# Kernel optimization log

Measured on AMD Instinct MI355X. Metric: run time of the kernel, lower is better.

Reference implementation:

```python
import jax, jax.numpy as jnp
import numpy as np

# Static configuration (mirrors init_kwargs / forward defaults)
KERNEL = 128          # WW
INDEX_BACK = 32768    # number of highest-frequency bins discarded
PADDING = 0           # padding_count (padding=None in forward)

def next_power2(x):
    return int(2 ** np.ceil(np.log2(x)))

def setup_inputs() -> dict:
    key = jax.random.key(0)
    k1, k2, k3 = jax.random.split(key, 3)
    N, C, W = 32, 8, 65536
    F = 16
    x = jax.random.normal(k1, (N, C, W), dtype=jnp.float32)
    weight = jax.random.normal(k2, (F, C, KERNEL), dtype=jnp.float32) * 0.1
    bias = jax.random.normal(k3, (F,), dtype=jnp.float32)
    return {"x": x, "weight": weight, "bias": bias}

def reference(x, weight, bias):
    # x: [N, C, W], weight: [F, C, WW], bias: [F]
    N, C, W = x.shape
    F, _, WW = weight.shape
    pad = PADDING
    out_W = W - WW + 1 + 2 * pad
    # fft size sized to also hold the backward dout correlation, then next pow2
    init_fft_size_input = W + 2 * pad + 2 * (WW - 1)
    init_fft_size_dout = out_W + 2 * (WW - 1)
    init_fft_size = next_power2(max(init_fft_size_input, init_fft_size_dout))
    half = init_fft_size // 2 + 1

    # rfft with implicit zero-padding to init_fft_size (input left-padded by `pad`)
    x_p = jnp.pad(x, ((0, 0), (0, 0), (pad, 0)))
    xfft = jnp.fft.rfft(x_p, n=init_fft_size, axis=-1)      # [N, C, half]
    yfft = jnp.fft.rfft(weight, n=init_fft_size, axis=-1)   # [F, C, half]

    # spectral compression: drop the INDEX_BACK highest-frequency bins
    keep = half - INDEX_BACK
    xfft = xfft[..., :keep]
    yfft = yfft[..., :keep]

    # cross-correlation in frequency domain (torch conv == correlation),
    # summing over input channels C in the spectrum (linearity of irfft)
    outfft = jnp.einsum('nck,fck->nfk', xfft, jnp.conj(yfft))  # [N, F, keep]

    # zero-pad discarded high frequencies back and invert
    outfft = jnp.pad(outfft, ((0, 0), (0, 0), (0, half - keep)))
    out = jnp.fft.irfft(outfft, n=init_fft_size, axis=-1)[..., :out_W]  # [N, F, out_W]

    out = out + bias[None, :, None]
    return out
```

## Files before the change

### kernel.cpp

```cpp
#include <hip/hip_runtime.h>

namespace {

constexpr int NFFT  = 65536;
constexpr int KEEPK = 32768;
constexpr int OUTW  = 65409;
constexpr size_t YBYTES = (size_t)128 * 32769 * 8;

typedef float2 cplx;

__device__ __forceinline__ cplx cmk(float x, float y){ return make_float2(x, y); }
__device__ __forceinline__ cplx cadd(cplx a, cplx b){ return cmk(a.x+b.x, a.y+b.y); }
__device__ __forceinline__ cplx csub(cplx a, cplx b){ return cmk(a.x-b.x, a.y-b.y); }
__device__ __forceinline__ cplx cmul(cplx a, cplx b){ return cmk(a.x*b.x - a.y*b.y, a.x*b.y + a.y*b.x); }
__device__ __forceinline__ cplx cmulj(cplx a, cplx b){
  return cmk(a.x*b.x + a.y*b.y, a.y*b.x - a.x*b.y); }

template<int DIR>
__device__ __forceinline__ void dft16(cplx v[16]) {
  const float C1 = 0.92387953251128674f;
  const float S1 = 0.38268343236508977f;
  const float C2 = 0.70710678118654752f;
  const float WR[16]  = {1.f, C1, C2, S1, 0.f, -S1, -C2, -C1, -1.f, -C1, -C2, -S1, 0.f, S1, C2, C1};
  const float WIF[16] = {0.f, -S1, -C2, -C1, -1.f, -C1, -C2, -S1, 0.f, S1, C2, C1, 1.f, C1, C2, S1};
  cplx s[16];
  #pragma unroll
  for (int n2 = 0; n2 < 4; ++n2) {
    cplx a = v[n2], b = v[n2+4], c = v[n2+8], d = v[n2+12];
    cplx ac = cadd(a,c), am = csub(a,c), bd = cadd(b,d), bm = csub(b,d);
    cplx x0 = cadd(ac, bd), x2 = csub(ac, bd), x1, x3;
    if (DIR == -1) { x1 = cmk(am.x + bm.y, am.y - bm.x); x3 = cmk(am.x - bm.y, am.y + bm.x); }
    else           { x1 = cmk(am.x - bm.y, am.y + bm.x); x3 = cmk(am.x + bm.y, am.y - bm.x); }
    s[0*4+n2] = x0;
    {
      int e1 = (n2*1) & 15, e2 = (n2*2) & 15, e3 = (n2*3) & 15;
      cplx w1 = cmk(WR[e1], (DIR==-1)? WIF[e1] : -WIF[e1]);
      cplx w2 = cmk(WR[e2], (DIR==-1)? WIF[e2] : -WIF[e2]);
      cplx w3 = cmk(WR[e3], (DIR==-1)? WIF[e3] : -WIF[e3]);
      s[1*4+n2] = cmul(x1, w1);
      s[2*4+n2] = cmul(x2, w2);
      s[3*4+n2] = cmul(x3, w3);
    }
  }
  #pragma unroll
  for (int t1 = 0; t1 < 4; ++t1) {
    cplx a = s[t1*4+0], b = s[t1*4+1], c = s[t1*4+2], d = s[t1*4+3];
    cplx ac = cadd(a,c), am = csub(a,c), bd = cadd(b,d), bm = csub(b,d);
    cplx x0 = cadd(ac,bd), x2 = csub(ac,bd), x1, x3;
    if (DIR == -1) { x1 = cmk(am.x + bm.y, am.y - bm.x); x3 = cmk(am.x - bm.y, am.y + bm.x); }
    else           { x1 = cmk(am.x - bm.y, am.y + bm.x); x3 = cmk(am.x + bm.y, am.y - bm.x); }
    v[t1+0] = x0; v[t1+4] = x1; v[t1+8] = x2; v[t1+12] = x3;
  }
}

template<int DIR>
__global__ __launch_bounds__(256)
void fft_pass_a(const cplx* __restrict__ in, long inStride, int inLen,
                cplx* __restrict__ T) {
  int blk = blockIdx.x;
  int seq = blk >> 4;
  int B0  = (blk & 15) << 4;
  int t = threadIdx.x;
  __shared__ cplx tile[16][260];
  {
    const cplx* src = in + (long)seq * inStride;
    int cb = t & 15, rg = t >> 4;
    #pragma unroll
    for (int i = 0; i < 16; ++i) {
      int a = i*16 + rg;
      int sIdx = a*256 + B0 + cb;
      cplx v = (sIdx < inLen) ? src[sIdx] : cmk(0.f, 0.f);
      tile[cb][a] = v;
    }
  }
  __syncthreads();
  int cc = t >> 4, j = t & 15;
  cplx x[16];
  #pragma unroll
  for (int a1 = 0; a1 < 16; ++a1) x[a1] = tile[cc][a1*16 + j];
  dft16<DIR>(x);
  {
    float sn, cs;
    __sincosf((float)DIR * 6.28318530717958648f * (float)j * (1.0f/256.0f), &sn, &cs);
    cplx r = cmk(cs, sn), cur = r;
    #pragma unroll
    for (int t1 = 1; t1 < 16; ++t1) { x[t1] = cmul(x[t1], cur); cur = cmul(cur, r); }
  }
  __syncthreads();
  #pragma unroll
  for (int t1 = 0; t1 < 16; ++t1) tile[cc][t1*16 + ((j + t1) & 15)] = x[t1];
  __syncthreads();
  #pragma unroll
  for (int a2 = 0; a2 < 16; ++a2) x[a2] = tile[cc][j*16 + ((a2 + j) & 15)];
  dft16<DIR>(x);
  int b = B0 + cc;
  cplx* dst = T + (long)seq * NFFT + (long)b * 256;
  {
    float sn, cs;
    __sincosf((float)DIR * 6.28318530717958648f * (float)(b*j) * (1.0f/65536.0f), &sn, &cs);
    cplx cur = cmk(cs, sn);
    __sincosf((float)DIR * 6.28318530717958648f * (float)b * (1.0f/4096.0f), &sn, &cs);
    cplx stp = cmk(cs, sn);
    #pragma unroll
    for (int t2 = 0; t2 < 16; ++t2) {
      dst[j + 16*t2] = cmul(x[t2], cur);
      cur = cmul(cur, stp);
    }
  }
}

template<int DIR, int MODE>
__global__ __launch_bounds__(256)
void fft_pass_b(const cplx* __restrict__ T, cplx* __restrict__ outZ,
                float* __restrict__ outR, const float* __restrict__ bias,
                int seqBase) {
  int blk = blockIdx.x;
  int seq = blk >> 4;
  int K0  = (blk & 15) << 4;
  int t = threadIdx.x;
  __shared__ cplx tile[16][260];
  {
    const cplx* src = T + (long)seq * NFFT;
    int ck = t & 15, rg = t >> 4;
    #pragma unroll
    for (int i = 0; i < 16; ++i) {
      int b = i*16 + rg;
      tile[ck][b] = src[b*256 + K0 + ck];
    }
  }
  __syncthreads();
  int cc = t >> 4, j = t & 15;
  cplx x[16];
  #pragma unroll
  for (int a1 = 0; a1 < 16; ++a1) x[a1] = tile[cc][a1*16 + j];
  dft16<DIR>(x);
  {
    float sn, cs;
    __sincosf((float)DIR * 6.28318530717958648f * (float)j * (1.0f/256.0f), &sn, &cs);
    cplx r = cmk(cs, sn), cur = r;
    #pragma unroll
    for (int t1 = 1; t1 < 16; ++t1) { x[t1] = cmul(x[t1], cur); cur = cmul(cur, r); }
  }
  __syncthreads();
  #pragma unroll
  for (int t1 = 0; t1 < 16; ++t1) tile[cc][t1*16 + ((j + t1) & 15)] = x[t1];
  __syncthreads();
  #pragma unroll
  for (int a2 = 0; a2 < 16; ++a2) x[a2] = tile[cc][j*16 + ((a2 + j) & 15)];
  dft16<DIR>(x);
  __syncthreads();
  #pragma unroll
  for (int t2 = 0; t2 < 16; ++t2) tile[cc][j + 16*t2] = x[t2];
  __syncthreads();
  int ck2 = t & 15, rg2 = t >> 4;
  if (MODE == 0) {
    cplx* dst = outZ + (long)seq * NFFT + K0 + ck2;
    #pragma unroll
    for (int i = 0; i < 16; ++i) {
      int k2 = i*16 + rg2;
      dst[256*k2] = tile[ck2][k2];
    }
  } else {
    const float sc = 1.0f / 65536.0f;
    int gseq = seqBase + seq;
    float bf = bias[gseq & 15];
    float* dst = outR + (long)gseq * OUTW;
    #pragma unroll
    for (int i = 0; i < 16; ++i) {
      int k2 = i*16 + rg2;
      int s  = K0 + ck2 + 256*k2;
      int tp = 2*s;
      cplx v = tile[ck2][k2];
      if (tp < OUTW)     dst[tp]   = v.x * sc + bf;
      if (tp + 1 < OUTW) dst[tp+1] = v.y * sc + bf;
    }
  }
}

__global__ __launch_bounds__(256)
void weight_spec(const float* __restrict__ wgt, cplx* __restrict__ Y) {
  int seq = blockIdx.y;
  int k = blockIdx.x * 256 + threadIdx.x;
  __shared__ float wt[128];
  if (threadIdx.x < 128) wt[threadIdx.x] = wgt[seq * 128 + threadIdx.x];
  __syncthreads();
  if (k > KEEPK) return;
  float sn, cs;
  __sincosf(-3.14159265358979324f * (float)k * (1.0f/65536.0f), &sn, &cs);
  cplx r  = cmk(cs, sn);
  cplx r2 = cmul(r, r);
  cplx r4 = cmul(r2, r2);
  cplx r8 = cmul(r4, r4);
  cplx av[8];
  #pragma unroll
  for (int v = 0; v < 8; ++v) av[v] = cmk(0.f, 0.f);
  cplx C = cmk(1.f, 0.f);
  #pragma unroll
  for (int u = 0; u < 16; ++u) {
    #pragma unroll
    for (int v = 0; v < 8; ++v) {
      float w = wt[u*8 + v];
      av[v].x += w * C.x;
      av[v].y += w * C.y;
    }
    C = cmul(C, r8);
  }
  cplx acc = av[7];
  #pragma unroll
  for (int v = 6; v >= 0; --v) acc = cadd(av[v], cmul(r, acc));
  Y[(long)seq * 32769 + k] = acc;
}

__global__ __launch_bounds__(256)
void mac_pack(const cplx* __restrict__ Zx, const cplx* __restrict__ Yspec,
              cplx* __restrict__ Zout, int Bn) {
  int K0 = blockIdx.x * 32;
  int tid = threadIdx.x;
  int kk = tid & 31;
  int ng = tid >> 5;
  int k = K0 + kk;
  __shared__ cplx Yt[16][8][32];
  for (int e = tid; e < 16*8*32; e += 256) {
    int f = e >> 8;
    int c = (e >> 5) & 7;
    int q = e & 31;
    int kg = K0 + q;
    Yt[f][c][q] = (kg <= KEEPK) ? Yspec[(long)(f*8 + c) * 32769 + kg] : cmk(0.f, 0.f);
  }
  __syncthreads();
  if (k > KEEPK) return;
  float sn, cs;
  __sincosf(-3.14159265358979324f * (float)k * (1.0f/65536.0f), &sn, &cs);
  cplx w  = cmk(cs, sn);
  cplx wp = cmk(cs, -sn);
  int nPerG = (Bn + 7) >> 3;
  for (int nn = 0; nn < nPerG; ++nn) {
    int ln = ng * nPerG + nn;
    if (ln >= Bn) break;
    cplx X[8];
    #pragma unroll
    for (int c = 0; c < 8; ++c) {
      const cplx* Z = Zx + (long)(ln*8 + c) * NFFT;
      cplx zk = Z[k];
      cplx zm = Z[(NFFT - k) & (NFFT - 1)];
      cplx E = cmk(0.5f*(zk.x + zm.x), 0.5f*(zk.y - zm.y));
      cplx D = cmk(zk.x - zm.x, zk.y + zm.y);
      cplx O = cmk(0.5f*D.y, -0.5f*D.x);
      X[c] = cadd(E, cmul(w, O));
    }
    #pragma unroll
    for (int f = 0; f < 16; ++f) {
      cplx S = cmk(0.f, 0.f);
      #pragma unroll
      for (int c = 0; c < 8; ++c) S = cadd(S, cmulj(X[c], Yt[f][c][kk]));
      cplx* Zo = Zout + (long)(ln*16 + f) * NFFT;
      if (k == KEEPK) {
        Zo[k] = cmk(S.x, -S.y);
      } else {
        cplx E2 = cmk(0.5f*S.x, 0.5f*S.y);
        cplx O2 = cmul(wp, E2);
        Zo[k] = cmk(E2.x - O2.y, E2.y + O2.x);
        if (k > 0)
          Zo[NFFT - k] = cmk(E2.x + O2.y, O2.x - E2.y);
      }
    }
  }
}

}

extern "C" void kernel_launch(void* const* d_in, const int* in_sizes, int n_in,
                              void* d_out, int out_size, void* d_ws, size_t ws_size,
                              hipStream_t stream) {
  const cplx*  x    = (const cplx*)d_in[0];
  const float* wgt  = (const float*)d_in[1];
  const float* bias = (const float*)d_in[2];
  float* out = (float*)d_out;

  static const int BnOpt[5] = {16, 8, 4, 2, 1};
  int ti = 4;
  for (int i = 0; i < 5; ++i) {
    size_t zxb = (size_t)BnOpt[i] * 8  * NFFT * sizeof(cplx);
    size_t zob = (size_t)BnOpt[i] * 16 * NFFT * sizeof(cplx);
    if (YBYTES + zxb + 2 * zob <= ws_size) { ti = i; break; }
  }
  const int Bn = BnOpt[ti];
  const size_t zxb = (size_t)Bn * 8  * NFFT * sizeof(cplx);
  const size_t zob = (size_t)Bn * 16 * NFFT * sizeof(cplx);

  char* ws = (char*)d_ws;
  cplx* Y  = (cplx*)ws;
  cplx* Zx = (cplx*)(ws + YBYTES);
  cplx* Zo = (cplx*)(ws + YBYTES + zxb);
  cplx* T  = (cplx*)(ws + YBYTES + zxb + zob);

  weight_spec<<<dim3(129, 128), dim3(256), 0, stream>>>(wgt, Y);

  for (int n0 = 0; n0 < 32; n0 += Bn) {
    int sx = Bn * 8;
    int so = Bn * 16;
    fft_pass_a<-1><<<dim3(sx*16), dim3(256), 0, stream>>>(x + (long)n0*8*32768, 32768, 32768, T);
    fft_pass_b<-1,0><<<dim3(sx*16), dim3(256), 0, stream>>>(T, Zx, (float*)nullptr, (const float*)nullptr, 0);
    mac_pack<<<dim3(1025), dim3(256), 0, stream>>>(Zx, Y, Zo, Bn);
    fft_pass_a<1><<<dim3(so*16), dim3(256), 0, stream>>>(Zo, 65536, 65536, T);
    fft_pass_b<1,1><<<dim3(so*16), dim3(256), 0, stream>>>(T, (cplx*)nullptr, out, bias, n0*16);
  }
}
```

Measured before the change: 662.3 us.

## Fuse forward FFT pass B, spectral MAC and inverse FFT pass A into one kernel

```diff
diff --git a/kernel.cpp b/kernel.cpp
--- a/kernel.cpp
+++ b/kernel.cpp
@@ -3,9 +3,8 @@
 namespace {
 
 constexpr int NFFT  = 65536;
-constexpr int KEEPK = 32768;
 constexpr int OUTW  = 65409;
-constexpr size_t YBYTES = (size_t)128 * 32769 * 8;
+constexpr size_t Y2BYTES = (size_t)256 * 129 * 128 * 8;
 
 typedef float2 cplx;
 
@@ -94,7 +93,7 @@
   for (int a2 = 0; a2 < 16; ++a2) x[a2] = tile[cc][j*16 + ((a2 + j) & 15)];
   dft16<DIR>(x);
   int b = B0 + cc;
-  cplx* dst = T + (long)seq * NFFT + (long)b * 256;
+  cplx* dst = T + (long)seq * NFFT + b;
   {
     float sn, cs;
     __sincosf((float)DIR * 6.28318530717958648f * (float)(b*j) * (1.0f/65536.0f), &sn, &cs);
@@ -103,7 +102,7 @@
     cplx stp = cmk(cs, sn);
     #pragma unroll
     for (int t2 = 0; t2 < 16; ++t2) {
-      dst[j + 16*t2] = cmul(x[t2], cur);
+      dst[(j + 16*t2) * 256] = cmul(x[t2], cur);
       cur = cmul(cur, stp);
     }
   }
@@ -178,90 +177,199 @@
 }
 
 __global__ __launch_bounds__(256)
-void weight_spec(const float* __restrict__ wgt, cplx* __restrict__ Y) {
-  int seq = blockIdx.y;
-  int k = blockIdx.x * 256 + threadIdx.x;
-  __shared__ float wt[128];
-  if (threadIdx.x < 128) wt[threadIdx.x] = wgt[seq * 128 + threadIdx.x];
-  __syncthreads();
-  if (k > KEEPK) return;
-  float sn, cs;
-  __sincosf(-3.14159265358979324f * (float)k * (1.0f/65536.0f), &sn, &cs);
-  cplx r  = cmk(cs, sn);
-  cplx r2 = cmul(r, r);
-  cplx r4 = cmul(r2, r2);
-  cplx r8 = cmul(r4, r4);
-  cplx av[8];
-  #pragma unroll
-  for (int v = 0; v < 8; ++v) av[v] = cmk(0.f, 0.f);
-  cplx C = cmk(1.f, 0.f);
-  #pragma unroll
-  for (int u = 0; u < 16; ++u) {
-    #pragma unroll
-    for (int v = 0; v < 8; ++v) {
-      float w = wt[u*8 + v];
-      av[v].x += w * C.x;
-      av[v].y += w * C.y;
-    }
-    C = cmul(C, r8);
-  }
-  cplx acc = av[7];
-  #pragma unroll
-  for (int v = 6; v >= 0; --v) acc = cadd(av[v], cmul(r, acc));
-  Y[(long)seq * 32769 + k] = acc;
+void weight_spec(const float* __restrict__ wgt, cplx* __restrict__ Y2) {
+  const int k1 = blockIdx.x;
+  const int fg = blockIdx.y;
+  const int t  = threadIdx.x;
+  __shared__ float wt[16][129];
+  for (int e = t; e < 16*128; e += 256)
+    wt[e >> 7][e & 127] = wgt[(fg*16 + (e >> 7))*128 + (e & 127)];
+  __syncthreads();
+  const int fcL = t & 15;
+  const int fc  = fg*16 + fcL;
+  for (int m = t >> 4; m < 129; m += 16) {
+    int k = k1 + 256*m;
+    if (k > 32768) break;
+    float sn, cs;
+    __sincosf(-3.14159265358979324f * (float)k * (1.0f/65536.0f), &sn, &cs);
+    cplx r  = cmk(cs, sn);
+    cplx r2 = cmul(r, r);
+    cplx r4 = cmul(r2, r2);
+    cplx r8 = cmul(r4, r4);
+    cplx av[8];
+    #pragma unroll
+    for (int v = 0; v < 8; ++v) av[v] = cmk(0.f, 0.f);
+    cplx C = cmk(1.f, 0.f);
+    #pragma unroll
+    for (int u = 0; u < 16; ++u) {
+      #pragma unroll
+      for (int v = 0; v < 8; ++v) {
+        float w = wt[fcL][u*8 + v];
+        av[v].x += w * C.x;
+        av[v].y += w * C.y;
+      }
+      C = cmul(C, r8);
+    }
+    cplx acc = av[7];
+    #pragma unroll
+    for (int v = 6; v >= 0; --v) acc = cadd(av[v], cmul(r, acc));
+    Y2[((long)k1*129 + m)*128 + fc] = acc;
+  }
 }
 
 __global__ __launch_bounds__(256)
-void mac_pack(const cplx* __restrict__ Zx, const cplx* __restrict__ Yspec,
-              cplx* __restrict__ Zout, int Bn) {
-  int K0 = blockIdx.x * 32;
-  int tid = threadIdx.x;
-  int kk = tid & 31;
-  int ng = tid >> 5;
-  int k = K0 + kk;
-  __shared__ cplx Yt[16][8][32];
-  for (int e = tid; e < 16*8*32; e += 256) {
-    int f = e >> 8;
-    int c = (e >> 5) & 7;
-    int q = e & 31;
-    int kg = K0 + q;
-    Yt[f][c][q] = (kg <= KEEPK) ? Yspec[(long)(f*8 + c) * 32769 + kg] : cmk(0.f, 0.f);
-  }
-  __syncthreads();
-  if (k > KEEPK) return;
-  float sn, cs;
-  __sincosf(-3.14159265358979324f * (float)k * (1.0f/65536.0f), &sn, &cs);
-  cplx w  = cmk(cs, sn);
-  cplx wp = cmk(cs, -sn);
-  int nPerG = (Bn + 7) >> 3;
-  for (int nn = 0; nn < nPerG; ++nn) {
-    int ln = ng * nPerG + nn;
-    if (ln >= Bn) break;
-    cplx X[8];
-    #pragma unroll
-    for (int c = 0; c < 8; ++c) {
-      const cplx* Z = Zx + (long)(ln*8 + c) * NFFT;
-      cplx zk = Z[k];
-      cplx zm = Z[(NFFT - k) & (NFFT - 1)];
+void fused_mid(const cplx* __restrict__ T1, const cplx* __restrict__ Y2,
+               cplx* __restrict__ T2) {
+  const int ln  = blockIdx.x;
+  const int p   = blockIdx.y;
+  const int cLo = p;
+  const int cHi = (256 - p) & 255;
+  const bool selfp = (p == 0) || (p == 128);
+  const int t = threadIdx.x;
+  const int g = t >> 4;
+  const int j = t & 15;
+  const int c = g & 7;
+  const int half = g >> 3;
+  const int col = half ? cHi : cLo;
+
+  __shared__ cplx Ts[16][260];
+  __shared__ cplx Xs[8][2][130];
+
+  const float C16 = 0.98078528040323044913f;
+  const float S16 = 0.19509032201612826785f;
+
+  cplx x[16];
+  {
+    const cplx* src = T1 + ((long)(ln*8 + c) * NFFT + (long)col * 256);
+    #pragma unroll
+    for (int a1 = 0; a1 < 16; ++a1) x[a1] = src[a1*16 + j];
+  }
+  dft16<-1>(x);
+  {
+    float sn, cs;
+    __sincosf(-6.28318530717958648f * (float)j * (1.0f/256.0f), &sn, &cs);
+    cplx r = cmk(cs, sn), cur = r;
+    #pragma unroll
+    for (int t1 = 1; t1 < 16; ++t1) { x[t1] = cmul(x[t1], cur); cur = cmul(cur, r); }
+  }
+  #pragma unroll
+  for (int t1 = 0; t1 < 16; ++t1) Ts[g][t1*16 + ((j + t1) & 15)] = x[t1];
+  #pragma unroll
+  for (int a2 = 0; a2 < 16; ++a2) x[a2] = Ts[g][j*16 + ((a2 + j) & 15)];
+  dft16<-1>(x);
+  #pragma unroll
+  for (int t2 = 0; t2 < 16; ++t2) Ts[g][j + 16*t2] = x[t2];
+  __syncthreads();
+
+  {
+    float sn, cs;
+    __sincosf(-3.14159265358979324f * (float)(col + 256*j) * (1.0f/65536.0f), &sn, &cs);
+    cplx w = cmk(cs, sn);
+    const cplx stp = cmk(C16, -S16);
+    #pragma unroll
+    for (int t2 = 0; t2 < 8; ++t2) {
+      int m = j + 16*t2;
+      int k = col + 256*m;
+      cplx zk = x[t2];
+      int mi = (65536 - k) & 65535;
+      cplx zm = Ts[g ^ 8][mi >> 8];
       cplx E = cmk(0.5f*(zk.x + zm.x), 0.5f*(zk.y - zm.y));
       cplx D = cmk(zk.x - zm.x, zk.y + zm.y);
       cplx O = cmk(0.5f*D.y, -0.5f*D.x);
-      X[c] = cadd(E, cmul(w, O));
-    }
-    #pragma unroll
-    for (int f = 0; f < 16; ++f) {
-      cplx S = cmk(0.f, 0.f);
+      Xs[c][half][m] = cadd(E, cmul(w, O));
+      w = cmul(w, stp);
+    }
+  }
+  if (p == 0 && half == 0 && j == 0) {
+    cplx zk = x[8];
+    cplx X = cmk(zk.x, -zk.y);
+    Xs[c][0][128] = X;
+    Xs[c][1][128] = X;
+  }
+  __syncthreads();
+
+  const int f = g;
+  for (int r = 0; r < 2; ++r) {
+    if (r == 1 && selfp) break;
+    const int mcol = r ? cHi : cLo;
+    const int colP = (256 - mcol) & 255;
+    cplx z[16];
+    {
+      float sn, cs;
+      __sincosf(3.14159265358979324f * (float)(mcol + 256*j) * (1.0f/65536.0f), &sn, &cs);
+      cplx wp = cmk(cs, sn);
+      const cplx stp = cmk(C16, S16);
       #pragma unroll
-      for (int c = 0; c < 8; ++c) S = cadd(S, cmulj(X[c], Yt[f][c][kk]));
-      cplx* Zo = Zout + (long)(ln*16 + f) * NFFT;
-      if (k == KEEPK) {
-        Zo[k] = cmk(S.x, -S.y);
-      } else {
+      for (int t2 = 0; t2 < 8; ++t2) {
+        int m = j + 16*t2;
+        const float4* yv = reinterpret_cast<const float4*>(
+            Y2 + (((long)mcol*129 + m)*128 + f*8));
+        float4 y0 = yv[0], y1 = yv[1], y2 = yv[2], y3 = yv[3];
+        cplx S = cmulj(Xs[0][r][m], cmk(y0.x, y0.y));
+        S = cadd(S, cmulj(Xs[1][r][m], cmk(y0.z, y0.w)));
+        S = cadd(S, cmulj(Xs[2][r][m], cmk(y1.x, y1.y)));
+        S = cadd(S, cmulj(Xs[3][r][m], cmk(y1.z, y1.w)));
+        S = cadd(S, cmulj(Xs[4][r][m], cmk(y2.x, y2.y)));
+        S = cadd(S, cmulj(Xs[5][r][m], cmk(y2.z, y2.w)));
+        S = cadd(S, cmulj(Xs[6][r][m], cmk(y3.x, y3.y)));
+        S = cadd(S, cmulj(Xs[7][r][m], cmk(y3.z, y3.w)));
         cplx E2 = cmk(0.5f*S.x, 0.5f*S.y);
         cplx O2 = cmul(wp, E2);
-        Zo[k] = cmk(E2.x - O2.y, E2.y + O2.x);
-        if (k > 0)
-          Zo[NFFT - k] = cmk(E2.x + O2.y, O2.x - E2.y);
+        z[t2] = cmk(E2.x - O2.y, E2.y + O2.x);
+        wp = cmul(wp, stp);
+      }
+    }
+    {
+      int kp0 = 32768 - mcol - 256*j;
+      float sn, cs;
+      __sincosf(3.14159265358979324f * (float)kp0 * (1.0f/65536.0f), &sn, &cs);
+      cplx wq = cmk(cs, sn);
+      const cplx stp = cmk(C16, -S16);
+      #pragma unroll
+      for (int t2 = 8; t2 < 16; ++t2) {
+        int kp = kp0 - 4096*(t2 - 8);
+        int mm = kp >> 8;
+        const float4* yv = reinterpret_cast<const float4*>(
+            Y2 + (((long)colP*129 + mm)*128 + f*8));
+        float4 y0 = yv[0], y1 = yv[1], y2 = yv[2], y3 = yv[3];
+        cplx S = cmulj(Xs[0][1-r][mm], cmk(y0.x, y0.y));
+        S = cadd(S, cmulj(Xs[1][1-r][mm], cmk(y0.z, y0.w)));
+        S = cadd(S, cmulj(Xs[2][1-r][mm], cmk(y1.x, y1.y)));
+        S = cadd(S, cmulj(Xs[3][1-r][mm], cmk(y1.z, y1.w)));
+        S = cadd(S, cmulj(Xs[4][1-r][mm], cmk(y2.x, y2.y)));
+        S = cadd(S, cmulj(Xs[5][1-r][mm], cmk(y2.z, y2.w)));
+        S = cadd(S, cmulj(Xs[6][1-r][mm], cmk(y3.x, y3.y)));
+        S = cadd(S, cmulj(Xs[7][1-r][mm], cmk(y3.z, y3.w)));
+        cplx E2 = cmk(0.5f*S.x, 0.5f*S.y);
+        cplx O2 = cmul(wq, E2);
+        z[t2] = cmk(E2.x + O2.y, O2.x - E2.y);
+        wq = cmul(wq, stp);
+      }
+    }
+    dft16<1>(z);
+    {
+      float sn, cs;
+      __sincosf(6.28318530717958648f * (float)j * (1.0f/256.0f), &sn, &cs);
+      cplx rr = cmk(cs, sn), cur = rr;
+      #pragma unroll
+      for (int t1 = 1; t1 < 16; ++t1) { z[t1] = cmul(z[t1], cur); cur = cmul(cur, rr); }
+    }
+    #pragma unroll
+    for (int t1 = 0; t1 < 16; ++t1) Ts[g][t1*16 + ((j + t1) & 15)] = z[t1];
+    #pragma unroll
+    for (int a2 = 0; a2 < 16; ++a2) z[a2] = Ts[g][j*16 + ((a2 + j) & 15)];
+    dft16<1>(z);
+    {
+      float sn, cs;
+      __sincosf(6.28318530717958648f * (float)(mcol*j) * (1.0f/65536.0f), &sn, &cs);
+      cplx cur = cmk(cs, sn);
+      __sincosf(6.28318530717958648f * (float)mcol * (1.0f/4096.0f), &sn, &cs);
+      cplx stp = cmk(cs, sn);
+      cplx* dst = T2 + (long)(ln*16 + f) * NFFT + (long)mcol * 256;
+      #pragma unroll
+      for (int t2 = 0; t2 < 16; ++t2) {
+        dst[j + 16*t2] = cmul(z[t2], cur);
+        cur = cmul(cur, stp);
       }
     }
   }
@@ -278,31 +386,23 @@
   float* out = (float*)d_out;
 
   static const int BnOpt[5] = {16, 8, 4, 2, 1};
-  int ti = 4;
+  int Bn = 1;
   for (int i = 0; i < 5; ++i) {
-    size_t zxb = (size_t)BnOpt[i] * 8  * NFFT * sizeof(cplx);
-    size_t zob = (size_t)BnOpt[i] * 16 * NFFT * sizeof(cplx);
-    if (YBYTES + zxb + 2 * zob <= ws_size) { ti = i; break; }
-  }
-  const int Bn = BnOpt[ti];
-  const size_t zxb = (size_t)Bn * 8  * NFFT * sizeof(cplx);
-  const size_t zob = (size_t)Bn * 16 * NFFT * sizeof(cplx);
-
+    size_t need = Y2BYTES + (size_t)BnOpt[i] * 12582912ull;
+    if (need <= ws_size) { Bn = BnOpt[i]; break; }
+  }
   char* ws = (char*)d_ws;
-  cplx* Y  = (cplx*)ws;
-  cplx* Zx = (cplx*)(ws + YBYTES);
-  cplx* Zo = (cplx*)(ws + YBYTES + zxb);
-  cplx* T  = (cplx*)(ws + YBYTES + zxb + zob);
-
-  weight_spec<<<dim3(129, 128), dim3(256), 0, stream>>>(wgt, Y);
+  cplx* Y2 = (cplx*)ws;
+  cplx* T1 = (cplx*)(ws + Y2BYTES);
+  cplx* T2 = (cplx*)(ws + Y2BYTES + (size_t)Bn * 4194304ull);
+
+  weight_spec<<<dim3(256, 8), dim3(256), 0, stream>>>(wgt, Y2);
 
   for (int n0 = 0; n0 < 32; n0 += Bn) {
-    int sx = Bn * 8;
-    int so = Bn * 16;
-    fft_pass_a<-1><<<dim3(sx*16), dim3(256), 0, stream>>>(x + (long)n0*8*32768, 32768, 32768, T);
-    fft_pass_b<-1,0><<<dim3(sx*16), dim3(256), 0, stream>>>(T, Zx, (float*)nullptr, (const float*)nullptr, 0);
-    mac_pack<<<dim3(1025), dim3(256), 0, stream>>>(Zx, Y, Zo, Bn);
-    fft_pass_a<1><<<dim3(so*16), dim3(256), 0, stream>>>(Zo, 65536, 65536, T);
-    fft_pass_b<1,1><<<dim3(so*16), dim3(256), 0, stream>>>(T, (cplx*)nullptr, out, bias, n0*16);
-  }
-}
+    fft_pass_a<-1><<<dim3(Bn*8*16), dim3(256), 0, stream>>>(
+        x + (long)n0*8*32768, 32768, 32768, T1);
+    fused_mid<<<dim3(Bn, 129), dim3(256), 0, stream>>>(T1, Y2, T2);
+    fft_pass_b<1,1><<<dim3(Bn*16*16), dim3(256), 0, stream>>>(
+        T2, (cplx*)nullptr, out, bias, n0*16);
+  }
+}
```

After: 764.7 us. 1.15x slower.
